# Performance work log

Hardware: AMD Instinct MI355X
Metric: run time of the kernel (lower is better)

Reference implementation:

```python
import jax, jax.numpy as jnp
import numpy as np

D = 256      # dim_model
H = 8        # n_head
FFN = 1024
L = 2        # n_layers
WIN = 100.0  # window_size of LocalisedEncoding
MINWL = 0.01 # min_wavelength of LocalisedEncoding
EPS = 1e-5


def _mass_sinusoid(mz):
    # depthcharge MassEncoder: min_wavelength=0.001, max_wavelength=10000
    n_sin = D // 2
    n_cos = D - n_sin
    base = 0.001 / (2.0 * np.pi)
    scale = 10000.0 / 0.001
    sin_term = (base * scale ** (np.arange(n_sin) / (n_sin - 1))).astype(np.float32)
    cos_term = (base * scale ** (np.arange(n_cos) / (n_cos - 1))).astype(np.float32)
    return jnp.concatenate([jnp.sin(mz / sin_term), jnp.cos(mz / cos_term)], axis=-1)


def _pe_lookup(pe, mass):
    # LocalisedEncoding.forward: clamp, linear index into precomputed table
    m = jnp.clip(mass, -WIN, WIN)
    idx = ((m + 1.0 + WIN) / MINWL).astype(jnp.int32)
    return pe[idx]


def _ln(x, g, b):
    mu = jnp.mean(x, axis=-1, keepdims=True)
    var = jnp.mean((x - mu) ** 2, axis=-1, keepdims=True)
    return (x - mu) * jax.lax.rsqrt(var + EPS) * g + b


def _forward(spectra, pe, latent, int_w, in_w, in_b, out_w, out_b,
             l1_w, l1_b, l2_w, l2_b, n1_g, n1_b, n2_g, n2_b):
    B, Np, _ = spectra.shape
    pad = jnp.sum(spectra, axis=2) == 0  # padded peaks
    # CustomPeakEncoder with mass=None, precursor_mass=None, dim_intensity=None
    peaks = _mass_sinusoid(spectra[:, :, :1]) + spectra[:, :, 1:2] @ int_w.T
    x = jnp.concatenate([jnp.broadcast_to(latent, (B, 1, D)), peaks], axis=1)
    mask = jnp.concatenate([jnp.zeros((B, 1), bool), pad], axis=1)  # [B,N]
    masses = jnp.concatenate([jnp.zeros((B, 1), spectra.dtype), spectra[:, :, 0]], axis=1)
    N = Np + 1
    hd = D // H
    scale = 1.0 / np.sqrt(hd)
    neg = jnp.asarray(-1e9, x.dtype)

    for l in range(L):
        wq, wk, wv = in_w[l, :D], in_w[l, D:2 * D], in_w[l, 2 * D:]
        bq, bk, bv = in_b[l, :D], in_b[l, D:2 * D], in_b[l, 2 * D:]
        if l == 0:
            # localized path: relative mass-difference encoding added to K/V
            pe0 = _pe_lookup(pe, jnp.zeros((), x.dtype))          # [D]
            q_in = x + pe0                                         # [B,N,D]
            rel = masses[:, None, :] - masses[:, :, None]          # m_j - m_i, [B,N,N]
            kv_in = x[:, None, :, :] + _pe_lookup(pe, rel)         # [B,N,N,D]
            Q = (q_in @ wq.T + bq).reshape(B, N, H, hd)
            K = (kv_in @ wk.T + bk).reshape(B, N, N, H, hd)
            V = (kv_in @ wv.T + bv).reshape(B, N, N, H, hd)
            s = jnp.einsum('bihd,bijhd->bhij', Q, K) * scale
            s = jnp.where(mask[:, None, None, :], neg, s)
            a = jax.nn.softmax(s, axis=-1)
            y = jnp.einsum('bhij,bijhd->bihd', a, V).reshape(B, N, D)
        else:
            Q = (x @ wq.T + bq).reshape(B, N, H, hd)
            K = (x @ wk.T + bk).reshape(B, N, H, hd)
            V = (x @ wv.T + bv).reshape(B, N, H, hd)
            s = jnp.einsum('bihd,bjhd->bhij', Q, K) * scale
            s = jnp.where(mask[:, None, None, :], neg, s)
            a = jax.nn.softmax(s, axis=-1)
            y = jnp.einsum('bhij,bjhd->bihd', a, V).reshape(B, N, D)
        y = y @ out_w[l].T + out_b[l]
        x = _ln(x + y, n1_g[l], n1_b[l])
        f = jax.nn.relu(x @ l1_w[l].T + l1_b[l]) @ l2_w[l].T + l2_b[l]
        x = _ln(x + f, n2_g[l], n2_b[l])
    return x


def setup_inputs() -> dict:
    key = jax.random.key(0)
    ks = jax.random.split(key, 14)
    B, Np = 16, 150
    mz = jax.random.uniform(ks[0], (B, Np, 1), dtype=jnp.float32) * 300.0
    inten = jax.random.uniform(ks[1], (B, Np, 1), dtype=jnp.float32)
    spectra = jnp.concatenate([mz, inten], axis=-1)
    # zero-pad the last 20 peaks of every other spectrum
    pad = (jnp.arange(Np)[None, :] >= 130) & (jnp.arange(B)[:, None] % 2 == 0)
    spectra = jnp.where(pad[:, :, None], 0.0, spectra)

    # LocalisedEncoding precomputed pe buffer (casanovo_style=True)
    max_len = int((WIN + 1) * 2 / MINWL)  # 20200
    pos = np.arange(max_len) - max_len // 2
    div = np.exp(np.arange(0, D, 2) * (-np.log(10000.0) / D))
    pe_np = np.zeros((max_len, D), np.float32)
    pe_np[:, : D // 2] = np.sin(pos[:, None] * div)
    pe_np[:, D // 2:] = np.cos(pos[:, None] * div)

    s = 0.05
    return {
        'spectra': spectra,
        'pe': jnp.asarray(pe_np),
        'latent': jax.random.normal(ks[2], (1, 1, D), jnp.float32) * s,
        'int_w': jax.random.normal(ks[3], (D, 1), jnp.float32) * s,
        'in_w': jax.random.normal(ks[4], (L, 3 * D, D), jnp.float32) * s,
        'in_b': jax.random.normal(ks[5], (L, 3 * D), jnp.float32) * s,
        'out_w': jax.random.normal(ks[6], (L, D, D), jnp.float32) * s,
        'out_b': jax.random.normal(ks[7], (L, D), jnp.float32) * s,
        'l1_w': jax.random.normal(ks[8], (L, FFN, D), jnp.float32) * s,
        'l1_b': jax.random.normal(ks[9], (L, FFN), jnp.float32) * s,
        'l2_w': jax.random.normal(ks[10], (L, D, FFN), jnp.float32) * s,
        'l2_b': jax.random.normal(ks[11], (L, D), jnp.float32) * s,
        'n1_g': jnp.ones((L, D), jnp.float32),
        'n1_b': jnp.zeros((L, D), jnp.float32),
        'n2_g': jnp.ones((L, D), jnp.float32),
        'n2_b': jnp.zeros((L, D), jnp.float32),
    }


def reference(spectra, pe, latent, int_w, in_w, in_b, out_w, out_b,
              l1_w, l1_b, l2_w, l2_b, n1_g, n1_b, n2_g, n2_b):
    return _forward(spectra, pe, latent, int_w, in_w, in_b, out_w, out_b,
                    l1_w, l1_b, l2_w, l2_b, n1_g, n1_b, n2_g, n2_b)
```

## Files before the change

### kernel.cpp

```cpp
#include <hip/hip_runtime.h>
#include <hip/hip_bf16.h>
#include <math.h>

#define BB 16
#define NP 150
#define NN 151
#define DD 256
#define HH 8
#define HD 32
#define FFN_ 1024
#define PE_LEN 20200
#define ROWS (BB*NN)
#define MPAD 2432
#define PE_PAD 20224


typedef __attribute__((ext_vector_type(8))) short short8;
typedef __attribute__((ext_vector_type(4))) float f32x4;
typedef __attribute__((ext_vector_type(4))) unsigned u32x4;

#if defined(__has_builtin)
#if __has_builtin(__builtin_amdgcn_fdot2_f32_bf16)
#define HAVE_DOT2 1
#endif
#endif
#ifndef HAVE_DOT2
#define HAVE_DOT2 0
#endif

__device__ __forceinline__ float r16(float x) {
    return __bfloat162float(__float2bfloat16(x));
}
__device__ __forceinline__ float us2f(unsigned short u) {
    return __uint_as_float((unsigned)u << 16);
}
__device__ __forceinline__ float lo2f(unsigned x) {
    return __uint_as_float(x << 16);
}
__device__ __forceinline__ float hi2f(unsigned x) {
    return __uint_as_float(x & 0xFFFF0000u);
}
__device__ __forceinline__ unsigned cvtpk(float lo, float hi) {
    unsigned r;
    asm("v_cvt_pk_bf16_f32 %0, %1, %2" : "=v"(r) : "v"(lo), "v"(hi));
    return r;
}
#if HAVE_DOT2
typedef __attribute__((ext_vector_type(2))) __bf16 bf16x2;
__device__ __forceinline__ float dot2bf(unsigned a, unsigned b, float acc) {
    bf16x2 av = __builtin_bit_cast(bf16x2, a);
    bf16x2 bv = __builtin_bit_cast(bf16x2, b);
    return __builtin_amdgcn_fdot2_f32_bf16(av, bv, acc, false);
}
#endif

#define PACK_BLOCKS 1024
__global__ __launch_bounds__(256) void buildpack_kernel(
    const float* __restrict__ spectra, const float* __restrict__ latent,
    const float* __restrict__ int_w, const float* __restrict__ pe,
    float* __restrict__ x, __hip_bfloat16* __restrict__ xb,
    __hip_bfloat16* __restrict__ xqb,
    float* __restrict__ masses, float* __restrict__ maskf,
    const float* __restrict__ in_w,  __hip_bfloat16* __restrict__ inw_p,
    const float* __restrict__ out_w, __hip_bfloat16* __restrict__ outw_p,
    const float* __restrict__ l1_w,  __hip_bfloat16* __restrict__ l1w_p,
    const float* __restrict__ l2_w,  __hip_bfloat16* __restrict__ l2w_p,
    __hip_bfloat16* __restrict__ pe_p)
{
    int tid = threadIdx.x;
    if (blockIdx.x < ROWS) {
        int bn = blockIdx.x;
        int b = bn / NN, n = bn % NN;
        float val;
        if (n == 0) {
            val = latent[tid];
            if (tid == 0) { masses[bn] = 0.0f; maskf[bn] = 0.0f; }
        } else {
            float mz = spectra[(b*NP + n - 1)*2 + 0];
            float it = spectra[(b*NP + n - 1)*2 + 1];
            int i = (tid < 128) ? tid : tid - 128;
            const double base_d = 0.001 / (2.0 * 3.141592653589793);
            double term_d = base_d * pow(1.0e7, (double)i / 127.0);
            float tf = (float)term_d;
            double arg = (double)mz / (double)tf;
            double sv = (tid < 128) ? sin(arg) : cos(arg);
            val = (float)sv + it * int_w[tid];
            if (tid == 0) {
                masses[bn] = mz;
                maskf[bn] = ((mz + it) == 0.0f) ? 1.0f : 0.0f;
            }
        }
        x[bn*DD + tid] = val;
        xb[bn*DD + tid] = __float2bfloat16(val);
        xqb[bn*DD + tid] = __float2bfloat16(val + pe[10100*DD + tid]);
    } else {
        long long base = (long long)(blockIdx.x - ROWS) * 256 + tid;
        const long long stride = (long long)PACK_BLOCKS * 256;
        for (long long i = base; i < (long long)PE_PAD*DD; i += stride)
            pe_p[i] = __float2bfloat16(i < (long long)PE_LEN*DD ? pe[i] : 0.0f);
        for (long long i = base; i < 2LL*768*DD; i += stride)
            inw_p[i] = __float2bfloat16(in_w[i]);
        for (long long i = base; i < 2LL*DD*DD; i += stride)
            outw_p[i] = __float2bfloat16(out_w[i]);
        for (long long i = base; i < 2LL*FFN_*DD; i += stride)
            l1w_p[i] = __float2bfloat16(l1_w[i]);
        for (long long i = base; i < 2LL*DD*FFN_; i += stride)
            l2w_p[i] = __float2bfloat16(l2_w[i]);
    }
}

template<typename CT>
__global__ __launch_bounds__(256) void gemm_mfma(
    const __hip_bfloat16* __restrict__ A, const __hip_bfloat16* __restrict__ W,
    const float* __restrict__ bias, CT* __restrict__ C,
    int M, int Nc, int K, int ldc, int relu)
{
    int wave = threadIdx.x >> 6;
    int lane = threadIdx.x & 63;
    int NT = Nc >> 5;
    int MT = (M + 31) >> 5;
    int id = blockIdx.x * 4 + wave;
    if (id >= MT * NT) return;
    int mt = id / NT, nt = id % NT;
    int m0 = mt * 32, n0 = nt * 32;
    int rl = lane & 15, q8 = (lane >> 4) * 8;

    const short8* Ap0 = (const short8*)(A + (size_t)(m0 + rl)*K + q8);
    const short8* Ap1 = (const short8*)(A + (size_t)(m0 + 16 + rl)*K + q8);
    const short8* Wp0 = (const short8*)(W + (size_t)(n0 + rl)*K + q8);
    const short8* Wp1 = (const short8*)(W + (size_t)(n0 + 16 + rl)*K + q8);

    f32x4 acc00 = {0,0,0,0}, acc01 = {0,0,0,0};
    f32x4 acc10 = {0,0,0,0}, acc11 = {0,0,0,0};
    int steps = K >> 5;
    for (int s = 0; s < steps; ++s) {
        short8 a0 = Ap0[s*4];
        short8 a1 = Ap1[s*4];
        short8 b0 = Wp0[s*4];
        short8 b1 = Wp1[s*4];
        acc00 = __builtin_amdgcn_mfma_f32_16x16x32_bf16(a0, b0, acc00, 0, 0, 0);
        acc01 = __builtin_amdgcn_mfma_f32_16x16x32_bf16(a0, b1, acc01, 0, 0, 0);
        acc10 = __builtin_amdgcn_mfma_f32_16x16x32_bf16(a1, b0, acc10, 0, 0, 0);
        acc11 = __builtin_amdgcn_mfma_f32_16x16x32_bf16(a1, b1, acc11, 0, 0, 0);
    }

    int rbase = (lane >> 4) * 4;
    #pragma unroll
    for (int sm = 0; sm < 2; ++sm) {
        #pragma unroll
        for (int sn = 0; sn < 2; ++sn) {
            f32x4 a = (sm == 0) ? (sn == 0 ? acc00 : acc01)
                                : (sn == 0 ? acc10 : acc11);
            int gc = n0 + sn*16 + rl;
            float bv = bias ? r16(bias[gc]) : 0.0f;
            #pragma unroll
            for (int rg = 0; rg < 4; ++rg) {
                int gr = m0 + sm*16 + rbase + rg;
                if (gr < M) {
                    float val = r16(a[rg]);
                    if (bias) val = r16(val + bv);
                    if (relu) val = fmaxf(val, 0.0f);
                    C[(size_t)gr*ldc + gc] = (CT)val;
                }
            }
        }
    }
}

template<int K>
__global__ __launch_bounds__(256) void gemm_skinny(
    const __hip_bfloat16* __restrict__ A, const __hip_bfloat16* __restrict__ W,
    const float* __restrict__ bias, float* __restrict__ C,
    int M, int Nc, int ldc)
{
    int NT = Nc >> 5;
    int id = blockIdx.x;
    int mt = id / NT, nt = id % NT;
    int m0 = mt * 16, n0 = nt * 32;
    int wave = threadIdx.x >> 6;
    int lane = threadIdx.x & 63;
    int rl = lane & 15, q8 = (lane >> 4) * 8;
    const int K4 = K >> 2;
    int k0 = wave * K4;

    const short8* Ap  = (const short8*)(A + (size_t)(m0 + rl)*K + k0 + q8);
    const short8* Wp0 = (const short8*)(W + (size_t)(n0 + rl)*K + k0 + q8);
    const short8* Wp1 = (const short8*)(W + (size_t)(n0 + 16 + rl)*K + k0 + q8);

    f32x4 acc0 = {0,0,0,0}, acc1 = {0,0,0,0};
    #pragma unroll
    for (int s = 0; s < K4/32; ++s) {
        short8 a  = Ap[s*4];
        short8 b0 = Wp0[s*4];
        short8 b1 = Wp1[s*4];
        acc0 = __builtin_amdgcn_mfma_f32_16x16x32_bf16(a, b0, acc0, 0, 0, 0);
        acc1 = __builtin_amdgcn_mfma_f32_16x16x32_bf16(a, b1, acc1, 0, 0, 0);
    }

    __shared__ float red[4][8][65];
    #pragma unroll
    for (int rg = 0; rg < 4; ++rg) {
        red[wave][rg][lane]   = acc0[rg];
        red[wave][4+rg][lane] = acc1[rg];
    }
    __syncthreads();

    #pragma unroll
    for (int t = 0; t < 2; ++t) {
        int sl = wave*2 + t;
        float s = red[0][sl][lane] + red[1][sl][lane]
                + red[2][sl][lane] + red[3][sl][lane];
        int rg = sl & 3, sn = sl >> 2;
        int gr = m0 + (lane >> 4)*4 + rg;
        int gc = n0 + sn*16 + rl;
        float val = r16(s);
        val = r16(val + r16(bias[gc]));
        if (gr < M) C[(size_t)gr*ldc + gc] = val;
    }
}

#define PEKV_BLK 632u
#define QKV0_BLK 456u

__device__ __forceinline__ void pekv_body(
    unsigned bid, int wave, int lane,
    const __hip_bfloat16* __restrict__ A, const __hip_bfloat16* __restrict__ W,
    __hip_bfloat16* __restrict__ C)
{
    const int K = 256, Nc = 512, ldc = 512, M = PE_LEN;
    int NT = Nc >> 5;
    int MT4 = (M + 127) >> 7;
    int id = bid * 4 + wave;
    if (id >= MT4 * NT) return;
    int mt = id / NT, nt = id % NT;
    int m0 = mt * 128, n0 = nt * 32;
    int rl = lane & 15, q8 = (lane >> 4) * 8;

    const short8* Ab  = (const short8*)(A + (size_t)(m0 + rl)*K + q8);
    const short8* Wp0 = (const short8*)(W + (size_t)(n0 + rl)*K + q8);
    const short8* Wp1 = (const short8*)(W + (size_t)(n0 + 16 + rl)*K + q8);
    const int rstep = K >> 3;

    f32x4 acc[4][2][2] = {};
    for (int s = 0; s < 8; ++s) {
        short8 b0 = Wp0[s*4];
        short8 b1 = Wp1[s*4];
        short8 a[4][2];
        #pragma unroll
        for (int t = 0; t < 4; ++t) {
            a[t][0] = Ab[(size_t)(t*32)*rstep + s*4];
            a[t][1] = Ab[(size_t)(t*32+16)*rstep + s*4];
        }
        #pragma unroll
        for (int t = 0; t < 4; ++t) {
            acc[t][0][0] = __builtin_amdgcn_mfma_f32_16x16x32_bf16(a[t][0], b0, acc[t][0][0], 0, 0, 0);
            acc[t][0][1] = __builtin_amdgcn_mfma_f32_16x16x32_bf16(a[t][0], b1, acc[t][0][1], 0, 0, 0);
            acc[t][1][0] = __builtin_amdgcn_mfma_f32_16x16x32_bf16(a[t][1], b0, acc[t][1][0], 0, 0, 0);
            acc[t][1][1] = __builtin_amdgcn_mfma_f32_16x16x32_bf16(a[t][1], b1, acc[t][1][1], 0, 0, 0);
        }
    }

    int rbase = (lane >> 4) * 4;
    #pragma unroll
    for (int t = 0; t < 4; ++t) {
        #pragma unroll
        for (int sm = 0; sm < 2; ++sm) {
            #pragma unroll
            for (int sn = 0; sn < 2; ++sn) {
                f32x4 a = acc[t][sm][sn];
                int gc = n0 + sn*16 + rl;
                #pragma unroll
                for (int rg = 0; rg < 4; ++rg) {
                    int gr = m0 + t*32 + sm*16 + rbase + rg;
                    if (gr < M)
                        C[(size_t)gr*ldc + gc] = (__hip_bfloat16)r16(a[rg]);
                }
            }
        }
    }
}

__device__ __forceinline__ void qkv0_body(
    unsigned bid, int wave, int lane,
    const __hip_bfloat16* __restrict__ xqb, const __hip_bfloat16* __restrict__ xb,
    const __hip_bfloat16* __restrict__ inw_p, const float* __restrict__ in_b,
    __hip_bfloat16* __restrict__ qb, __hip_bfloat16* __restrict__ kvb, int M)
{
    int MT = (M + 31) >> 5;
    int id = bid * 4 + wave;
    if (id >= MT * 24) return;
    int mt = id / 24, ntt = id % 24;
    bool isQ = (ntt < 8);
    const __hip_bfloat16* A = isQ ? xqb : xb;
    const __hip_bfloat16* W = inw_p + (isQ ? (size_t)ntt*32*DD
                                           : (size_t)(256 + (ntt-8)*32)*DD);
    const float* bias = in_b + (isQ ? ntt*32 : 256 + (ntt-8)*32);
    __hip_bfloat16* C = isQ ? qb : kvb;
    int ldc = isQ ? 256 : 512;
    int cbase = isQ ? ntt*32 : (ntt-8)*32;
    int m0 = mt * 32;
    int rl = lane & 15, q8 = (lane >> 4) * 8;
    const int K = DD;

    const short8* Ap0 = (const short8*)(A + (size_t)(m0 + rl)*K + q8);
    const short8* Ap1 = (const short8*)(A + (size_t)(m0 + 16 + rl)*K + q8);
    const short8* Wp0 = (const short8*)(W + (size_t)(rl)*K + q8);
    const short8* Wp1 = (const short8*)(W + (size_t)(16 + rl)*K + q8);

    f32x4 acc00 = {0,0,0,0}, acc01 = {0,0,0,0};
    f32x4 acc10 = {0,0,0,0}, acc11 = {0,0,0,0};
    for (int s = 0; s < K/32; ++s) {
        short8 a0 = Ap0[s*4];
        short8 a1 = Ap1[s*4];
        short8 b0 = Wp0[s*4];
        short8 b1 = Wp1[s*4];
        acc00 = __builtin_amdgcn_mfma_f32_16x16x32_bf16(a0, b0, acc00, 0, 0, 0);
        acc01 = __builtin_amdgcn_mfma_f32_16x16x32_bf16(a0, b1, acc01, 0, 0, 0);
        acc10 = __builtin_amdgcn_mfma_f32_16x16x32_bf16(a1, b0, acc10, 0, 0, 0);
        acc11 = __builtin_amdgcn_mfma_f32_16x16x32_bf16(a1, b1, acc11, 0, 0, 0);
    }

    int rbase = (lane >> 4) * 4;
    #pragma unroll
    for (int sm = 0; sm < 2; ++sm) {
        #pragma unroll
        for (int sn = 0; sn < 2; ++sn) {
            f32x4 a = (sm == 0) ? (sn == 0 ? acc00 : acc01)
                                : (sn == 0 ? acc10 : acc11);
            int gc = cbase + sn*16 + rl;
            float bv = r16(bias[sn*16 + rl]);
            #pragma unroll
            for (int rg = 0; rg < 4; ++rg) {
                int gr = m0 + sm*16 + rbase + rg;
                if (gr < M) {
                    float val = r16(a[rg]);
                    val = r16(val + bv);
                    C[(size_t)gr*ldc + gc] = (__hip_bfloat16)val;
                }
            }
        }
    }
}

__global__ __launch_bounds__(256) void pekv_qkv0_kernel(
    const __hip_bfloat16* __restrict__ pe_p, const __hip_bfloat16* __restrict__ wkv0,
    __hip_bfloat16* __restrict__ pekv,
    const __hip_bfloat16* __restrict__ xqb, const __hip_bfloat16* __restrict__ xb,
    const __hip_bfloat16* __restrict__ inw_p, const float* __restrict__ in_b,
    __hip_bfloat16* __restrict__ qb, __hip_bfloat16* __restrict__ kvb)
{
    int wave = threadIdx.x >> 6;
    int lane = threadIdx.x & 63;
    if (blockIdx.x < PEKV_BLK)
        pekv_body(blockIdx.x, wave, lane, pe_p, wkv0, pekv);
    else
        qkv0_body(blockIdx.x - PEKV_BLK, wave, lane, xqb, xb, inw_p, in_b,
                  qb, kvb, ROWS);
}

template<bool USE_PE, int QS, int KS, int VS>
__global__ __launch_bounds__(256) void attn_kernel(
    const __hip_bfloat16* __restrict__ qp,
    const __hip_bfloat16* __restrict__ kp,
    const __hip_bfloat16* __restrict__ vp,
    const __hip_bfloat16* __restrict__ pekv,
    const float* __restrict__ masses, const float* __restrict__ maskf,
    __hip_bfloat16* __restrict__ yb)
{
    int b = blockIdx.x & 15;
    int i = blockIdx.x >> 4;
    int tid = threadIdx.x;
    int c = tid & 31;
    int g = tid >> 5;
    int h = c >> 2;

    __shared__ float sc[HH][152];
    __shared__ float msh[152];
    __shared__ int   tj[152];
    __shared__ __align__(16) float part[8][264];

    if (tid < NN) {
        msh[tid] = maskf[b*NN + tid];
        if (USE_PE) {
            double m = (double)masses[b*NN + tid] - (double)masses[b*NN + i];
            m = fmin(fmax(m, -100.0), 100.0);
            tj[tid] = (int)(((m + 1.0) + 100.0) / 0.01);
        }
    }

    unsigned qw[4];
    {
        const u32x4 q4 = *(const u32x4*)((const unsigned short*)qp
                            + (size_t)(b*NN + i)*QS + c*8);
        qw[0] = q4[0]; qw[1] = q4[1]; qw[2] = q4[2]; qw[3] = q4[3];
    }
#if !HAVE_DOT2
    float qf[8];
    #pragma unroll
    for (int w = 0; w < 4; ++w) { qf[2*w] = lo2f(qw[w]); qf[2*w+1] = hi2f(qw[w]); }
#endif
    __syncthreads();

    const float scale = 0.17677669529663687f;
    const unsigned short* kbase = (const unsigned short*)kp + (size_t)(b*NN)*KS + c*8;
    const unsigned short* vbase = (const unsigned short*)vp + (size_t)(b*NN)*VS + c*8;
    const unsigned short* pkb = (const unsigned short*)pekv + c*8;
    const unsigned short* pvb = (const unsigned short*)pekv + 256 + c*8;

    {
        int j = g;
        u32x4 kcur = *(const u32x4*)(kbase + (size_t)j*KS);
        u32x4 pcur;
        if (USE_PE) pcur = *(const u32x4*)(pkb + (size_t)tj[j]*512);
        for (int p = 0; p < 19; ++p) {
            int jn = j + 8;
            bool more = (jn < NN);
            u32x4 kn, pn;
            if (more) {
                kn = *(const u32x4*)(kbase + (size_t)jn*KS);
                if (USE_PE) pn = *(const u32x4*)(pkb + (size_t)tj[jn]*512);
            }
            float acc = 0.0f;
#if HAVE_DOT2
            #pragma unroll
            for (int w = 0; w < 4; ++w) {
                unsigned kd = kcur[w];
                if (USE_PE) {
                    unsigned pd = pcur[w];
                    float s0 = lo2f(kd) + lo2f(pd);
                    float s1 = hi2f(kd) + hi2f(pd);
                    kd = cvtpk(s0, s1);
                }
                acc = dot2bf(qw[w], kd, acc);
            }
#else
            #pragma unroll
            for (int w = 0; w < 4; ++w) {
                unsigned kd = kcur[w];
                float k0 = lo2f(kd), k1 = hi2f(kd);
                if (USE_PE) {
                    unsigned pd = pcur[w];
                    k0 = r16(k0 + lo2f(pd));
                    k1 = r16(k1 + hi2f(pd));
                }
                acc = fmaf(qf[2*w], k0, acc);
                acc = fmaf(qf[2*w+1], k1, acc);
            }
#endif
            acc += __shfl_xor(acc, 1);
            acc += __shfl_xor(acc, 2);
            if ((c & 3) == 0) {
                float s = acc * scale;
                if (msh[j] != 0.0f) s = -1e9f;
                sc[h][j] = s;
            }
            if (!more) break;
            j = jn; kcur = kn;
            if (USE_PE) pcur = pn;
        }
    }
    __syncthreads();

    {
        int lane = tid & 31;
        int hh = g;
        float mx = -INFINITY;
        for (int j = lane; j < NN; j += 32) mx = fmaxf(mx, sc[hh][j]);
        #pragma unroll
        for (int off = 16; off; off >>= 1) mx = fmaxf(mx, __shfl_xor(mx, off, 32));
        float sum = 0.0f;
        for (int j = lane; j < NN; j += 32) {
            float e = expf(sc[hh][j] - mx);
            sc[hh][j] = e;
            sum += e;
        }
        #pragma unroll
        for (int off = 16; off; off >>= 1) sum += __shfl_xor(sum, off, 32);
        float inv = 1.0f / sum;
        for (int j = lane; j < NN; j += 32) sc[hh][j] = r16(sc[hh][j] * inv);
    }
    __syncthreads();

    {
        float ya[8];
        #pragma unroll
        for (int u = 0; u < 8; ++u) ya[u] = 0.0f;

#if HAVE_DOT2
        u32x4 vA = *(const u32x4*)(vbase + (size_t)g*VS);
        u32x4 vB = *(const u32x4*)(vbase + (size_t)(g+8)*VS);
        u32x4 pA, pB;
        if (USE_PE) {
            pA = *(const u32x4*)(pvb + (size_t)tj[g]*512);
            pB = *(const u32x4*)(pvb + (size_t)tj[g+8]*512);
        }
        for (int t = 0; t < 9; ++t) {
            int jA = g + t*16, jB = jA + 8;
            u32x4 nvA, nvB, npA, npB;
            if (t < 8) {
                int nA = jA + 16, nB = jB + 16;
                nvA = *(const u32x4*)(vbase + (size_t)nA*VS);
                nvB = *(const u32x4*)(vbase + (size_t)nB*VS);
                if (USE_PE) {
                    npA = *(const u32x4*)(pvb + (size_t)tj[nA]*512);
                    npB = *(const u32x4*)(pvb + (size_t)tj[nB]*512);
                }
            }
            unsigned apair = cvtpk(sc[h][jA], sc[h][jB]);
            #pragma unroll
            for (int w = 0; w < 4; ++w) {
                unsigned lopair, hipair;
                if (USE_PE) {
                    float sA0 = lo2f(vA[w]) + lo2f(pA[w]);
                    float sA1 = hi2f(vA[w]) + hi2f(pA[w]);
                    float sB0 = lo2f(vB[w]) + lo2f(pB[w]);
                    float sB1 = hi2f(vB[w]) + hi2f(pB[w]);
                    lopair = cvtpk(sA0, sB0);
                    hipair = cvtpk(sA1, sB1);
                } else {
                    lopair = __builtin_amdgcn_perm(vB[w], vA[w], 0x05040100u);
                    hipair = __builtin_amdgcn_perm(vB[w], vA[w], 0x07060302u);
                }
                ya[2*w]   = dot2bf(apair, lopair, ya[2*w]);
                ya[2*w+1] = dot2bf(apair, hipair, ya[2*w+1]);
            }
            if (t < 8) {
                vA = nvA; vB = nvB;
                if (USE_PE) { pA = npA; pB = npB; }
            }
        }
        if (g + 144 < NN) {
            int jT = g + 144;
            u32x4 v = *(const u32x4*)(vbase + (size_t)jT*VS);
            u32x4 pq;
            if (USE_PE) pq = *(const u32x4*)(pvb + (size_t)tj[jT]*512);
            float aT = sc[h][jT];
            #pragma unroll
            for (int w = 0; w < 4; ++w) {
                float v0 = lo2f(v[w]), v1 = hi2f(v[w]);
                if (USE_PE) {
                    unsigned pk2 = cvtpk(v0 + lo2f(pq[w]), v1 + hi2f(pq[w]));
                    v0 = lo2f(pk2); v1 = hi2f(pk2);
                }
                ya[2*w]   = fmaf(aT, v0, ya[2*w]);
                ya[2*w+1] = fmaf(aT, v1, ya[2*w+1]);
            }
        }
#else
        int j = g;
        u32x4 vcur = *(const u32x4*)(vbase + (size_t)j*VS);
        u32x4 pcur;
        if (USE_PE) pcur = *(const u32x4*)(pvb + (size_t)tj[j]*512);
        float acur = sc[h][j];
        for (int p = 0; p < 19; ++p) {
            int jn = j + 8;
            bool more = (jn < NN);
            u32x4 vn, pn;
            float an = 0.0f;
            if (more) {
                vn = *(const u32x4*)(vbase + (size_t)jn*VS);
                if (USE_PE) pn = *(const u32x4*)(pvb + (size_t)tj[jn]*512);
                an = sc[h][jn];
            }
            #pragma unroll
            for (int w = 0; w < 4; ++w) {
                float v0 = lo2f(vcur[w]), v1 = hi2f(vcur[w]);
                if (USE_PE) {
                    v0 = r16(v0 + lo2f(pcur[w]));
                    v1 = r16(v1 + hi2f(pcur[w]));
                }
                ya[2*w]   = fmaf(acur, v0, ya[2*w]);
                ya[2*w+1] = fmaf(acur, v1, ya[2*w+1]);
            }
            if (!more) break;
            j = jn; vcur = vn; acur = an;
            if (USE_PE) pcur = pn;
        }
#endif
        f32x4* pp = (f32x4*)&part[g][c*8];
        pp[0] = f32x4{ya[0], ya[1], ya[2], ya[3]};
        pp[1] = f32x4{ya[4], ya[5], ya[6], ya[7]};
    }
    __syncthreads();

    {
        float s = part[0][tid];
        #pragma unroll
        for (int g2 = 1; g2 < 8; ++g2) s += part[g2][tid];
        yb[(size_t)(b*NN + i)*DD + tid] = __float2bfloat16(s);
    }
}

template<bool WRITE_B>
__global__ __launch_bounds__(256) void add_ln_kernel(
    const float* __restrict__ xin, const float* __restrict__ res,
    const float* __restrict__ g, const float* __restrict__ bb,
    float* __restrict__ xout, __hip_bfloat16* __restrict__ xbout)
{
    int r = blockIdx.x; int tid = threadIdx.x;
    float v = xin[r*DD + tid] + res[r*DD + tid];
    __shared__ float red[4];
    float s = v;
    #pragma unroll
    for (int off = 32; off; off >>= 1) s += __shfl_xor(s, off);
    if ((tid & 63) == 0) red[tid >> 6] = s;
    __syncthreads();
    float mu = (red[0] + red[1] + red[2] + red[3]) * (1.0f/256.0f);
    __syncthreads();
    float d = v - mu;
    float s2 = d*d;
    #pragma unroll
    for (int off = 32; off; off >>= 1) s2 += __shfl_xor(s2, off);
    if ((tid & 63) == 0) red[tid >> 6] = s2;
    __syncthreads();
    float var = (red[0] + red[1] + red[2] + red[3]) * (1.0f/256.0f);
    float out = d * (1.0f / sqrtf(var + 1e-5f)) * g[tid] + bb[tid];
    xout[r*DD + tid] = out;
    if (WRITE_B) xbout[r*DD + tid] = __float2bfloat16(out);
}

extern "C" void kernel_launch(void* const* d_in, const int* in_sizes, int n_in,
                              void* d_out, int out_size, void* d_ws, size_t ws_size,
                              hipStream_t stream)
{
    const float* spectra = (const float*)d_in[0];
    const float* pe      = (const float*)d_in[1];
    const float* latent  = (const float*)d_in[2];
    const float* int_w   = (const float*)d_in[3];
    const float* in_w    = (const float*)d_in[4];
    const float* in_b    = (const float*)d_in[5];
    const float* out_w   = (const float*)d_in[6];
    const float* out_b   = (const float*)d_in[7];
    const float* l1_w    = (const float*)d_in[8];
    const float* l1_b    = (const float*)d_in[9];
    const float* l2_w    = (const float*)d_in[10];
    const float* l2_b    = (const float*)d_in[11];
    const float* n1_g    = (const float*)d_in[12];
    const float* n1_b    = (const float*)d_in[13];
    const float* n2_g    = (const float*)d_in[14];
    const float* n2_b    = (const float*)d_in[15];

    float* x      = (float*)d_ws;
    float* y2     = x      + ROWS*DD;
    float* masses = y2     + ROWS*DD;
    float* maskf  = masses + ROWS;
    __hip_bfloat16* bp = (__hip_bfloat16*)(maskf + ROWS);
    __hip_bfloat16* xb    = bp;  bp += (size_t)MPAD*DD;
    __hip_bfloat16* xqb   = bp;  bp += (size_t)MPAD*DD;
    __hip_bfloat16* qb    = bp;  bp += (size_t)MPAD*DD;
    __hip_bfloat16* kvb   = bp;  bp += (size_t)MPAD*768;
    __hip_bfloat16* yb    = bp;  bp += (size_t)MPAD*DD;
    __hip_bfloat16* f1b   = bp;  bp += (size_t)MPAD*FFN_;
    __hip_bfloat16* pekv  = bp;  bp += (size_t)PE_PAD*512;
    __hip_bfloat16* pe_p  = bp;  bp += (size_t)PE_PAD*DD;
    __hip_bfloat16* inw_p = bp;  bp += (size_t)2*768*DD;
    __hip_bfloat16* outw_p= bp;  bp += (size_t)2*DD*DD;
    __hip_bfloat16* l1w_p = bp;  bp += (size_t)2*FFN_*DD;
    __hip_bfloat16* l2w_p = bp;  bp += (size_t)2*DD*FFN_;

    dim3 blk(256);
    auto GG = [](int M, int Nc){ return dim3((unsigned)((((M+31)>>5)*(Nc>>5) + 3) / 4)); };
    const unsigned SKINNY = (ROWS/16) * (256 >> 5);

    buildpack_kernel<<<ROWS + PACK_BLOCKS, blk, 0, stream>>>(
        spectra, latent, int_w, pe, x, xb, xqb, masses, maskf,
        in_w, inw_p, out_w, outw_p, l1_w, l1w_p, l2_w, l2w_p, pe_p);

    pekv_qkv0_kernel<<<PEKV_BLK + QKV0_BLK, blk, 0, stream>>>(
        pe_p, inw_p + 256*DD, pekv, xqb, xb, inw_p, in_b, qb, kvb);

    attn_kernel<true,256,512,512><<<ROWS, blk, 0, stream>>>(
        qb, kvb, kvb + 256, pekv, masses, maskf, yb);
    gemm_skinny<256><<<SKINNY, blk, 0, stream>>>(
        yb, outw_p, out_b, y2, ROWS, 256, 256);
    add_ln_kernel<true><<<ROWS, blk, 0, stream>>>(x, y2, n1_g, n1_b, x, xb);
    gemm_mfma<__hip_bfloat16><<<GG(ROWS, 1024), blk, 0, stream>>>(
        xb, l1w_p, l1_b, f1b, ROWS, 1024, 256, 1024, 1);
    gemm_skinny<1024><<<SKINNY, blk, 0, stream>>>(
        f1b, l2w_p, l2_b, y2, ROWS, 256, 256);
    add_ln_kernel<true><<<ROWS, blk, 0, stream>>>(x, y2, n2_g, n2_b, x, xb);

    gemm_mfma<__hip_bfloat16><<<GG(ROWS, 768), blk, 0, stream>>>(
        xb, inw_p + 768*DD, in_b + 768, kvb, ROWS, 768, 256, 768, 0);
    attn_kernel<false,768,768,768><<<ROWS, blk, 0, stream>>>(
        kvb, kvb + 256, kvb + 512, nullptr, masses, maskf, yb);
    gemm_skinny<256><<<SKINNY, blk, 0, stream>>>(
        yb, outw_p + 256*DD, out_b + 256, y2, ROWS, 256, 256);
    add_ln_kernel<true><<<ROWS, blk, 0, stream>>>(x, y2, n1_g + 256, n1_b + 256, x, xb);
    gemm_mfma<__hip_bfloat16><<<GG(ROWS, 1024), blk, 0, stream>>>(
        xb, l1w_p + FFN_*DD, l1_b + 1024, f1b, ROWS, 1024, 256, 1024, 1);
    gemm_skinny<1024><<<SKINNY, blk, 0, stream>>>(
        f1b, l2w_p + DD*FFN_, l2_b + 256, y2, ROWS, 256, 256);
    add_ln_kernel<false><<<ROWS, blk, 0, stream>>>(x, y2, n2_g + 256, n2_b + 256,
                                                   (float*)d_out, nullptr);
}
```

Baseline: 304.0 us.

## Split fused PE/QKV0 GEMM launch and deepen attention K/V prefetch

The combined pe-kv and layer-0 QKV kernel is split back into two separate launches. In the attention kernel the K/PE and V/PE register prefetch pipelines go from one step ahead to two steps ahead, so more global-memory latency is hidden behind the dot-product work. The trade-off is an extra kernel launch, which serialises two GEMMs that could previously share the GPU, plus higher register pressure in the attention kernel.

Result: slower. 314.4 us (+3.4%).

```diff
diff --git a/kernel.cpp b/kernel.cpp
--- a/kernel.cpp
+++ b/kernel.cpp
@@ -219,18 +219,16 @@
     }
 }
 
-#define PEKV_BLK 632u
-#define QKV0_BLK 456u
-
-__device__ __forceinline__ void pekv_body(
-    unsigned bid, int wave, int lane,
+__global__ __launch_bounds__(256) void gemm_pekv(
     const __hip_bfloat16* __restrict__ A, const __hip_bfloat16* __restrict__ W,
-    __hip_bfloat16* __restrict__ C)
-{
-    const int K = 256, Nc = 512, ldc = 512, M = PE_LEN;
+    __hip_bfloat16* __restrict__ C, int M, int Nc, int ldc)
+{
+    const int K = 256;
+    int wave = threadIdx.x >> 6;
+    int lane = threadIdx.x & 63;
     int NT = Nc >> 5;
     int MT4 = (M + 127) >> 7;
-    int id = bid * 4 + wave;
+    int id = blockIdx.x * 4 + wave;
     if (id >= MT4 * NT) return;
     int mt = id / NT, nt = id % NT;
     int m0 = mt * 128, n0 = nt * 32;
@@ -280,14 +278,15 @@
     }
 }
 
-__device__ __forceinline__ void qkv0_body(
-    unsigned bid, int wave, int lane,
+__global__ __launch_bounds__(256) void gemm_qkv0(
     const __hip_bfloat16* __restrict__ xqb, const __hip_bfloat16* __restrict__ xb,
     const __hip_bfloat16* __restrict__ inw_p, const float* __restrict__ in_b,
     __hip_bfloat16* __restrict__ qb, __hip_bfloat16* __restrict__ kvb, int M)
 {
+    int wave = threadIdx.x >> 6;
+    int lane = threadIdx.x & 63;
     int MT = (M + 31) >> 5;
-    int id = bid * 4 + wave;
+    int id = blockIdx.x * 4 + wave;
     if (id >= MT * 24) return;
     int mt = id / 24, ntt = id % 24;
     bool isQ = (ntt < 8);
@@ -342,22 +341,6 @@
     }
 }
 
-__global__ __launch_bounds__(256) void pekv_qkv0_kernel(
-    const __hip_bfloat16* __restrict__ pe_p, const __hip_bfloat16* __restrict__ wkv0,
-    __hip_bfloat16* __restrict__ pekv,
-    const __hip_bfloat16* __restrict__ xqb, const __hip_bfloat16* __restrict__ xb,
-    const __hip_bfloat16* __restrict__ inw_p, const float* __restrict__ in_b,
-    __hip_bfloat16* __restrict__ qb, __hip_bfloat16* __restrict__ kvb)
-{
-    int wave = threadIdx.x >> 6;
-    int lane = threadIdx.x & 63;
-    if (blockIdx.x < PEKV_BLK)
-        pekv_body(blockIdx.x, wave, lane, pe_p, wkv0, pekv);
-    else
-        qkv0_body(blockIdx.x - PEKV_BLK, wave, lane, xqb, xb, inw_p, in_b,
-                  qb, kvb, ROWS);
-}
-
 template<bool USE_PE, int QS, int KS, int VS>
 __global__ __launch_bounds__(256) void attn_kernel(
     const __hip_bfloat16* __restrict__ qp,
@@ -408,38 +391,40 @@
     const unsigned short* pvb = (const unsigned short*)pekv + 256 + c*8;
 
     {
-        int j = g;
-        u32x4 kcur = *(const u32x4*)(kbase + (size_t)j*KS);
-        u32x4 pcur;
-        if (USE_PE) pcur = *(const u32x4*)(pkb + (size_t)tj[j]*512);
+        u32x4 kA = *(const u32x4*)(kbase + (size_t)g*KS);
+        u32x4 kB = *(const u32x4*)(kbase + (size_t)(g+8)*KS);
+        u32x4 pA, pB;
+        if (USE_PE) {
+            pA = *(const u32x4*)(pkb + (size_t)tj[g]*512);
+            pB = *(const u32x4*)(pkb + (size_t)tj[g+8]*512);
+        }
         for (int p = 0; p < 19; ++p) {
-            int jn = j + 8;
-            bool more = (jn < NN);
-            u32x4 kn, pn;
-            if (more) {
-                kn = *(const u32x4*)(kbase + (size_t)jn*KS);
-                if (USE_PE) pn = *(const u32x4*)(pkb + (size_t)tj[jn]*512);
+            int j = g + p*8;
+            if (j >= NN) break;
+            int jf = j + 16;
+            u32x4 kC, pC;
+            if (jf < NN) {
+                kC = *(const u32x4*)(kbase + (size_t)jf*KS);
+                if (USE_PE) pC = *(const u32x4*)(pkb + (size_t)tj[jf]*512);
             }
             float acc = 0.0f;
 #if HAVE_DOT2
             #pragma unroll
             for (int w = 0; w < 4; ++w) {
-                unsigned kd = kcur[w];
+                unsigned kd = kA[w];
                 if (USE_PE) {
-                    unsigned pd = pcur[w];
-                    float s0 = lo2f(kd) + lo2f(pd);
-                    float s1 = hi2f(kd) + hi2f(pd);
-                    kd = cvtpk(s0, s1);
+                    unsigned pd = pA[w];
+                    kd = cvtpk(lo2f(kd) + lo2f(pd), hi2f(kd) + hi2f(pd));
                 }
                 acc = dot2bf(qw[w], kd, acc);
             }
 #else
             #pragma unroll
             for (int w = 0; w < 4; ++w) {
-                unsigned kd = kcur[w];
+                unsigned kd = kA[w];
                 float k0 = lo2f(kd), k1 = hi2f(kd);
                 if (USE_PE) {
-                    unsigned pd = pcur[w];
+                    unsigned pd = pA[w];
                     k0 = r16(k0 + lo2f(pd));
                     k1 = r16(k1 + hi2f(pd));
                 }
@@ -454,9 +439,8 @@
                 if (msh[j] != 0.0f) s = -1e9f;
                 sc[h][j] = s;
             }
-            if (!more) break;
-            j = jn; kcur = kn;
-            if (USE_PE) pcur = pn;
+            kA = kB; kB = kC;
+            if (USE_PE) { pA = pB; pB = pC; }
         }
     }
     __syncthreads();
@@ -487,23 +471,27 @@
         for (int u = 0; u < 8; ++u) ya[u] = 0.0f;
 
 #if HAVE_DOT2
-        u32x4 vA = *(const u32x4*)(vbase + (size_t)g*VS);
-        u32x4 vB = *(const u32x4*)(vbase + (size_t)(g+8)*VS);
-        u32x4 pA, pB;
+        u32x4 vA0 = *(const u32x4*)(vbase + (size_t)g*VS);
+        u32x4 vB0 = *(const u32x4*)(vbase + (size_t)(g+8)*VS);
+        u32x4 vA1 = *(const u32x4*)(vbase + (size_t)(g+16)*VS);
+        u32x4 vB1 = *(const u32x4*)(vbase + (size_t)(g+24)*VS);
+        u32x4 pA0, pB0, pA1, pB1;
         if (USE_PE) {
-            pA = *(const u32x4*)(pvb + (size_t)tj[g]*512);
-            pB = *(const u32x4*)(pvb + (size_t)tj[g+8]*512);
+            pA0 = *(const u32x4*)(pvb + (size_t)tj[g]*512);
+            pB0 = *(const u32x4*)(pvb + (size_t)tj[g+8]*512);
+            pA1 = *(const u32x4*)(pvb + (size_t)tj[g+16]*512);
+            pB1 = *(const u32x4*)(pvb + (size_t)tj[g+24]*512);
         }
         for (int t = 0; t < 9; ++t) {
             int jA = g + t*16, jB = jA + 8;
-            u32x4 nvA, nvB, npA, npB;
-            if (t < 8) {
-                int nA = jA + 16, nB = jB + 16;
-                nvA = *(const u32x4*)(vbase + (size_t)nA*VS);
-                nvB = *(const u32x4*)(vbase + (size_t)nB*VS);
+            u32x4 vA2, vB2, pA2, pB2;
+            if (t + 2 <= 8) {
+                int nA = jA + 32, nB = jB + 32;
+                vA2 = *(const u32x4*)(vbase + (size_t)nA*VS);
+                vB2 = *(const u32x4*)(vbase + (size_t)nB*VS);
                 if (USE_PE) {
-                    npA = *(const u32x4*)(pvb + (size_t)tj[nA]*512);
-                    npB = *(const u32x4*)(pvb + (size_t)tj[nB]*512);
+                    pA2 = *(const u32x4*)(pvb + (size_t)tj[nA]*512);
+                    pB2 = *(const u32x4*)(pvb + (size_t)tj[nB]*512);
                 }
             }
             unsigned apair = cvtpk(sc[h][jA], sc[h][jB]);
@@ -511,23 +499,21 @@
             for (int w = 0; w < 4; ++w) {
                 unsigned lopair, hipair;
                 if (USE_PE) {
-                    float sA0 = lo2f(vA[w]) + lo2f(pA[w]);
-                    float sA1 = hi2f(vA[w]) + hi2f(pA[w]);
-                    float sB0 = lo2f(vB[w]) + lo2f(pB[w]);
-                    float sB1 = hi2f(vB[w]) + hi2f(pB[w]);
+                    float sA0 = lo2f(vA0[w]) + lo2f(pA0[w]);
+                    float sA1 = hi2f(vA0[w]) + hi2f(pA0[w]);
+                    float sB0 = lo2f(vB0[w]) + lo2f(pB0[w]);
+                    float sB1 = hi2f(vB0[w]) + hi2f(pB0[w]);
                     lopair = cvtpk(sA0, sB0);
                     hipair = cvtpk(sA1, sB1);
                 } else {
-                    lopair = __builtin_amdgcn_perm(vB[w], vA[w], 0x05040100u);
-                    hipair = __builtin_amdgcn_perm(vB[w], vA[w], 0x07060302u);
+                    lopair = __builtin_amdgcn_perm(vB0[w], vA0[w], 0x05040100u);
+                    hipair = __builtin_amdgcn_perm(vB0[w], vA0[w], 0x07060302u);
                 }
                 ya[2*w]   = dot2bf(apair, lopair, ya[2*w]);
                 ya[2*w+1] = dot2bf(apair, hipair, ya[2*w+1]);
             }
-            if (t < 8) {
-                vA = nvA; vB = nvB;
-                if (USE_PE) { pA = npA; pB = npB; }
-            }
+            vA0 = vA1; vB0 = vB1; vA1 = vA2; vB1 = vB2;
+            if (USE_PE) { pA0 = pA1; pB0 = pB1; pA1 = pA2; pB1 = pB2; }
         }
         if (g + 144 < NN) {
             int jT = g + 144;
@@ -660,14 +646,21 @@
 
     dim3 blk(256);
     auto GG = [](int M, int Nc){ return dim3((unsigned)((((M+31)>>5)*(Nc>>5) + 3) / 4)); };
+    const unsigned STRIPS = (ROWS + 31) / 32;
     const unsigned SKINNY = (ROWS/16) * (256 >> 5);
 
     buildpack_kernel<<<ROWS + PACK_BLOCKS, blk, 0, stream>>>(
         spectra, latent, int_w, pe, x, xb, xqb, masses, maskf,
         in_w, inw_p, out_w, outw_p, l1_w, l1w_p, l2_w, l2w_p, pe_p);
 
-    pekv_qkv0_kernel<<<PEKV_BLK + QKV0_BLK, blk, 0, stream>>>(
-        pe_p, inw_p + 256*DD, pekv, xqb, xb, inw_p, in_b, qb, kvb);
+    {
+        unsigned mt4 = (PE_LEN + 127) >> 7;
+        unsigned tiles = mt4 * (512 >> 5);
+        gemm_pekv<<<dim3((tiles + 3) / 4), blk, 0, stream>>>(
+            pe_p, inw_p + 256*DD, pekv, PE_LEN, 512, 512);
+    }
+    gemm_qkv0<<<dim3((STRIPS*24 + 3)/4), blk, 0, stream>>>(
+        xqb, xb, inw_p, in_b, qb, kvb, ROWS);
 
     attn_kernel<true,256,512,512><<<ROWS, blk, 0, stream>>>(
         qb, kvb, kvb + 256, pekv, masses, maskf, yb);
```
